# Kernel optimization log

Hardware: AMD Instinct MI355X
Metric: run time of the kernel (lower is better)

The kernel has to match this reference:

```python
import jax, jax.numpy as jnp
import numpy as np

NUM_HEADS = 16
WINDOW = 128

def setup_inputs() -> dict:
    key = jax.random.key(0)
    ks = jax.random.split(key, 9)
    E, B, S = 1024, 2, 2048
    sc = 1.0 / np.sqrt(E)
    return {
        'x':  jax.random.normal(ks[0], (B, S, E), jnp.float32),
        'Wq': jax.random.normal(ks[1], (E, E), jnp.float32) * sc,
        'bq': jax.random.normal(ks[2], (E,), jnp.float32) * 0.02,
        'Wk': jax.random.normal(ks[3], (E, E), jnp.float32) * sc,
        'bk': jax.random.normal(ks[4], (E,), jnp.float32) * 0.02,
        'Wv': jax.random.normal(ks[5], (E, E), jnp.float32) * sc,
        'bv': jax.random.normal(ks[6], (E,), jnp.float32) * 0.02,
        'Wo': jax.random.normal(ks[7], (E, E), jnp.float32) * sc,
        'bo': jax.random.normal(ks[8], (E,), jnp.float32) * 0.02,
    }

def reference(x, Wq, bq, Wk, bk, Wv, bv, Wo, bo):
    B, S, E = x.shape
    H = NUM_HEADS
    D = E // H
    # projections -> [B, H, S, D]
    q = (x @ Wq + bq).reshape(B, S, H, D).transpose(0, 2, 1, 3)
    k = (x @ Wk + bk).reshape(B, S, H, D).transpose(0, 2, 1, 3)
    v = (x @ Wv + bv).reshape(B, S, H, D).transpose(0, 2, 1, 3)
    # dense scores [B, H, S, S]
    energy = jnp.einsum('bhqd,bhkd->bhqk', q, k)
    idx = jnp.arange(S)
    blocked = jnp.abs(idx[:, None] - idx[None, :]) > WINDOW  # True = outside band
    neg = jnp.finfo(jnp.float32).min
    energy = jnp.where(blocked[None, None], neg, energy)
    # note: original scales by sqrt(emb_size), not sqrt(head_dim)
    att = jax.nn.softmax(energy / jnp.sqrt(jnp.float32(E)), axis=-1)
    out = jnp.einsum('bhqk,bhkd->bhqd', att, v)
    out = out.transpose(0, 2, 1, 3).reshape(B, S, E)
    return out @ Wo + bo
```

## Files before the change

kernel.cpp:

```cpp
#include <hip/hip_runtime.h>

typedef unsigned short u16;
typedef unsigned int u32;
typedef __attribute__((ext_vector_type(8))) short bf16x8;
typedef __attribute__((ext_vector_type(4))) float f32x4;
typedef __attribute__((ext_vector_type(4))) unsigned int u32x4;
typedef __attribute__((ext_vector_type(4))) unsigned short u16x4;

#define DEV static __device__ __forceinline__

DEV u16 f2bf(float f) {
  unsigned u = __builtin_bit_cast(unsigned, f);
  u += 0x7FFFu + ((u >> 16) & 1u);
  return (u16)(u >> 16);
}

DEV u32 cvt_pk_bf16(float lo, float hi) {
  u32 d;
  asm("v_cvt_pk_bf16_f32 %0, %1, %2" : "=v"(d) : "v"(lo), "v"(hi));
  return d;
}

DEV void load_lds16(const void* g, void* l) {
  __builtin_amdgcn_global_load_lds(
      (const __attribute__((address_space(1))) unsigned int*)g,
      (__attribute__((address_space(3))) unsigned int*)l, 16, 0, 0);
}


__global__ void k_prep(const float* __restrict__ x,
                       const float* __restrict__ bq, const float* __restrict__ bk,
                       const float* __restrict__ bv,
                       const float* __restrict__ Wq, const float* __restrict__ Wk,
                       const float* __restrict__ Wv, const float* __restrict__ Wo,
                       u16* __restrict__ xb, u16* __restrict__ wtqkv,
                       u16* __restrict__ wto, float* __restrict__ bias) {
  const int tid = threadIdx.x;
  const int bid = blockIdx.x;
  if (bid < 4096) {
    __shared__ float t[32][33];
    const int wi = bid >> 10, inner = bid & 1023;
    const float* W = (wi == 0) ? Wq : (wi == 1) ? Wk : (wi == 2) ? Wv : Wo;
    u16* Wt = (wi == 3) ? wto : wtqkv + (size_t)wi * 1024 * 1024;
    const int tx = tid & 31, ty = tid >> 5;
    const int c0 = (inner & 31) * 32, r0 = (inner >> 5) * 32;
#pragma unroll
    for (int i = 0; i < 4; ++i)
      t[ty + i * 8][tx] = W[(size_t)(r0 + ty + i * 8) * 1024 + c0 + tx];
    __syncthreads();
#pragma unroll
    for (int i = 0; i < 4; ++i)
      Wt[(size_t)(c0 + ty + i * 8) * 1024 + r0 + tx] = f2bf(t[tx][ty + i * 8]);
  } else if (bid < 8192) {
    int i = ((bid - 4096) * 256 + tid) * 4;
    f32x4 v = *(const f32x4*)(x + i);
    u16x4 o;
#pragma unroll
    for (int j = 0; j < 4; ++j) o[j] = f2bf(v[j]);
    *(u16x4*)(xb + i) = o;
  } else {
    int i = (bid - 8192) * 256 + tid;
    float v = (i < 1024) ? bq[i] : (i < 2048) ? bk[i - 1024] : bv[i - 2048];
    bias[i] = v;
  }
}


template <int BN, typename CT>
__launch_bounds__(256, 2) __global__
void k_gemm_bt(const u16* __restrict__ A, const u16* __restrict__ Bt,
               const float* __restrict__ bias, CT* __restrict__ C, int ldc,
               u16* __restrict__ vtp) {
  constexpr int BM = 128, BK = 64;
  constexpr int NJ = BN / 32;
  constexpr int EPW = BN / 2 + 4;
  constexpr int HALF = (BM + BN) * BK * 2;
  constexpr int LPS = BM / 32 + BN / 32;
  __shared__ __align__(16) char smem[2 * HALF];
  float (*ep)[16][EPW] = (float (*)[16][EPW])smem;

  const int tid = threadIdx.x;
  const int w = tid >> 6, lane = tid & 63, g = lane >> 4, n16 = lane & 15;
  const int wm = w >> 1, wn = w & 1;

  const int nbx = gridDim.x;
  const int flat = blockIdx.y * nbx + blockIdx.x;
  const int cpx = (nbx * gridDim.y) >> 3;
  const int swz = (flat & 7) * cpx + (flat >> 3);
  const int m0 = (swz / nbx) * BM, n0 = (swz % nbx) * BN;

#define STAGE(k0, bsel)                                                        \
  do {                                                                         \
    u16* lAb = (u16*)(smem + (bsel) * HALF);                                   \
    u16* lBb = lAb + BM * BK;                                                  \
    _Pragma("unroll")                                                          \
    for (int r = 0; r < BM / 32; ++r) {                                        \
      int s = r * 256 + tid;                                                   \
      int row = s >> 3, cc = (s & 7) ^ (row & 7);                              \
      load_lds16(A + (size_t)(m0 + row) * 1024 + (k0) + cc * 8, lAb + s * 8);  \
    }                                                                          \
    _Pragma("unroll")                                                          \
    for (int r = 0; r < BN / 32; ++r) {                                        \
      int s = r * 256 + tid;                                                   \
      int row = s >> 3, cc = (s & 7) ^ (row & 7);                              \
      load_lds16(Bt + (size_t)(n0 + row) * 1024 + (k0) + cc * 8, lBb + s * 8); \
    }                                                                          \
  } while (0)

  f32x4 acc[4][NJ] = {};
  STAGE(0, 0);
  STAGE(64, 1);
#pragma unroll 2
  for (int t = 0; t < 16; ++t) {
    const int buf = t & 1;
    if (t < 15) {
      asm volatile("s_waitcnt vmcnt(%0)" ::"n"(LPS) : "memory");
    } else {
      asm volatile("s_waitcnt vmcnt(0)" ::: "memory");
    }
    __builtin_amdgcn_s_barrier();
    const u16* lAb = (const u16*)(smem + buf * HALF);
    const u16* lBb = lAb + BM * BK;
    bf16x8 af[2][4], bfr[2][NJ];
#pragma unroll
    for (int kh = 0; kh < 2; ++kh) {
      const int csel = ((kh * 4 + g) ^ (n16 & 7)) * 8;
#pragma unroll
      for (int i = 0; i < 4; ++i)
        af[kh][i] = *(const bf16x8*)&lAb[(wm * 64 + i * 16 + n16) * 64 + csel];
#pragma unroll
      for (int j = 0; j < NJ; ++j)
        bfr[kh][j] = *(const bf16x8*)&lBb[(wn * (BN / 2) + j * 16 + n16) * 64 + csel];
    }
    asm volatile("s_waitcnt lgkmcnt(0)" ::: "memory");
    __builtin_amdgcn_s_barrier();
    if (t < 14) STAGE((t + 2) * 64, buf);
    __builtin_amdgcn_s_setprio(1);
#pragma unroll
    for (int kh = 0; kh < 2; ++kh)
#pragma unroll
      for (int i = 0; i < 4; ++i)
#pragma unroll
        for (int j = 0; j < NJ; ++j)
          acc[i][j] =
              __builtin_amdgcn_mfma_f32_16x16x32_bf16(af[kh][i], bfr[kh][j], acc[i][j], 0, 0, 0);
    __builtin_amdgcn_s_setprio(0);
  }
#undef STAGE
  __syncthreads();

  const int m_base = m0 + wm * 64, n_base = n0 + wn * (BN / 2);
  bool vmode = false;
  if constexpr (sizeof(CT) == 2 && BN == 128)
    vmode = (vtp != nullptr) && (n_base >= 2048);

#pragma unroll
  for (int i = 0; i < 4; ++i) {
#pragma unroll
    for (int j = 0; j < NJ; ++j) {
      float bv = bias[n_base + j * 16 + n16];
#pragma unroll
      for (int jj = 0; jj < 4; ++jj)
        ep[w][g * 4 + jj][j * 16 + n16] = acc[i][j][jj] + bv;
    }
    asm volatile("s_waitcnt lgkmcnt(0)" ::: "memory");
    if (vmode) {
      const int head = (n_base - 2048) >> 6;
      const int m_row0 = m_base + i * 16;
      const int bb = m_row0 >> 11, s0 = m_row0 & 2047;
      union { u16 a[16]; u32x4 v[2]; } pk;
#pragma unroll
      for (int r = 0; r < 16; ++r) pk.a[r] = f2bf(ep[w][r][lane]);
      size_t vrow = ((size_t)(bb * 16 + head) * 64 + lane) * 2048 + s0;
      *(u32x4*)(vtp + vrow) = pk.v[0];
      *(u32x4*)(vtp + vrow + 8) = pk.v[1];
    } else {
      constexpr int CPR = BN / 8;
      constexpr int P = 16 * CPR / 64;
#pragma unroll
      for (int p = 0; p < P; ++p) {
        int fl = p * 64 + lane;
        int row = fl / CPR, cc = (fl % CPR) * 4;
        f32x4 v = *(const f32x4*)&ep[w][row][cc];
        size_t off = (size_t)(m_base + i * 16 + row) * ldc + n_base + cc;
        if constexpr (sizeof(CT) == 2) {
          u16x4 o;
#pragma unroll
          for (int q = 0; q < 4; ++q) o[q] = f2bf(v[q]);
          *(u16x4*)(C + off) = o;
        } else {
          *(f32x4*)(C + off) = v;
        }
      }
    }
    asm volatile("s_waitcnt lgkmcnt(0)" ::: "memory");
  }
}


__launch_bounds__(256, 3) __global__
void k_attn(const u16* __restrict__ qkv, const u16* __restrict__ vt,
            u16* __restrict__ attn) {
  __shared__ __align__(16) u16 KV[20480];
  __shared__ __align__(16) u16 Ostg[4][16][64];
  const int tid = threadIdx.x;
  const int w = tid >> 6, lane = tid & 63, g = lane >> 4, n16 = lane & 15;
  const int bid = (blockIdx.x & 7) * 128 + (blockIdx.x >> 3);
  const int qt = bid & 31, h = (bid >> 5) & 15, b = bid >> 9;
  const int q0b = qt * 64;
  const int kvb = q0b - 128;
  const int q0 = q0b + w * 16;
  const int kv0 = q0 - 128;
  const int q = q0 + n16;
  const int bh = b * 16 + h;

  {
    const u16* kpart = qkv + (size_t)b * 2048 * 3072 + 1024 + h * 64;
#pragma unroll
    for (int i = 0; i < 10; ++i) {
      int c = i * 256 + tid;
      int r = c >> 3, sl = c & 7;
      int m = (r & 3) | (((r >> 3) & 1) << 2);
      int srcr = min(max(kvb + r, 0), 2047);
      load_lds16(kpart + (size_t)srcr * 3072 + (sl ^ m) * 8, &KV[c * 8]);
    }
  }

  const size_t rowQ = (size_t)(b * 2048 + q) * 3072 + h * 64;
  bf16x8 qf0 = *(const bf16x8*)(qkv + rowQ + g * 8);
  bf16x8 qf1 = *(const bf16x8*)(qkv + rowQ + 32 + g * 8);
  __syncthreads();

  const int kbase = 8 * (n16 >> 2) + (n16 & 3);
  const int wrel = 16 * w;
  f32x4 sv[18];
#pragma unroll
  for (int t = 0; t < 18; ++t) {
    int kr = wrel + 32 * (t >> 1) + 4 * (t & 1) + kbase;
    int krl = min(kr, 319);
    int p = (krl & 3) | (((krl >> 3) & 1) << 2);
    const u16* kp = &KV[krl * 64];
    bf16x8 kf0 = *(const bf16x8*)(kp + (g ^ p) * 8);
    bf16x8 kf1 = *(const bf16x8*)(kp + ((g + 4) ^ p) * 8);
    f32x4 s = {0.f, 0.f, 0.f, 0.f};
    s = __builtin_amdgcn_mfma_f32_16x16x32_bf16(kf0, qf0, s, 0, 0, 0);
    s = __builtin_amdgcn_mfma_f32_16x16x32_bf16(kf1, qf1, s, 0, 0, 0);
    sv[t] = s;
  }
  __syncthreads();

  {
    const u16* vpart = vt + (size_t)bh * 64 * 2048;
#pragma unroll
    for (int i = 0; i < 10; ++i) {
      int c = i * 256 + tid;
      int d = c / 40, cc = c - d * 40;
      int j = cc ^ (d & 7);
      int srck = min(max(kvb + j * 8, 0), 2040);
      load_lds16(vpart + (size_t)d * 2048 + srck, &KV[c * 8]);
    }
  }

  const float NEG = -__builtin_inff();
#pragma unroll
  for (int t = 0; t < 18; ++t) {
    int kb = kv0 + 32 * (t >> 1) + 4 * (t & 1) + 8 * g;
#pragma unroll
    for (int jj = 0; jj < 4; ++jj) {
      int k = kb + jj;
      bool ok = ((unsigned)k < 2048u) && ((unsigned)(q - k + 128) <= 256u);
      sv[t][jj] = ok ? sv[t][jj] : NEG;
    }
  }

  float mx = NEG;
#pragma unroll
  for (int t = 0; t < 18; ++t)
    mx = fmaxf(mx, fmaxf(fmaxf(sv[t][0], sv[t][1]), fmaxf(sv[t][2], sv[t][3])));
  mx = fmaxf(mx, __shfl_xor(mx, 16));
  mx = fmaxf(mx, __shfl_xor(mx, 32));

  const float c = 0.04508422017f;
  const float nmc = -mx * c;
  float sum = 0.f;
#pragma unroll
  for (int t = 0; t < 18; ++t)
#pragma unroll
    for (int jj = 0; jj < 4; ++jj) {
      float p = exp2f(fmaf(sv[t][jj], c, nmc));
      sv[t][jj] = p;
      sum += p;
    }
  sum += __shfl_xor(sum, 16);
  sum += __shfl_xor(sum, 32);
  const float inv = 1.f / sum;

  __syncthreads();

  f32x4 oacc[4] = {};
#pragma unroll
  for (int s = 0; s < 9; ++s) {
    union { u32 u[4]; bf16x8 v; } paf;
    paf.u[0] = cvt_pk_bf16(sv[2 * s][0], sv[2 * s][1]);
    paf.u[1] = cvt_pk_bf16(sv[2 * s][2], sv[2 * s][3]);
    paf.u[2] = cvt_pk_bf16(sv[2 * s + 1][0], sv[2 * s + 1][1]);
    paf.u[3] = cvt_pk_bf16(sv[2 * s + 1][2], sv[2 * s + 1][3]);
    int jc = min(2 * w + 4 * s + g, 39);
#pragma unroll
    for (int dt = 0; dt < 4; ++dt) {
      int d = dt * 16 + n16;
      bf16x8 vf = *(const bf16x8*)&KV[d * 320 + (jc ^ (d & 7)) * 8];
      oacc[dt] = __builtin_amdgcn_mfma_f32_16x16x32_bf16(paf.v, vf, oacc[dt], 0, 0, 0);
    }
  }

  float rs[4];
#pragma unroll
  for (int jj = 0; jj < 4; ++jj) rs[jj] = __shfl(inv, 4 * g + jj);

#pragma unroll
  for (int dt = 0; dt < 4; ++dt)
#pragma unroll
    for (int jj = 0; jj < 4; ++jj)
      Ostg[w][g * 4 + jj][dt * 16 + n16] = f2bf(oacc[dt][jj] * rs[jj]);
  asm volatile("s_waitcnt lgkmcnt(0)" ::: "memory");
#pragma unroll
  for (int p = 0; p < 2; ++p) {
    int fl = p * 512 + lane * 8;
    int row = fl >> 6, col = fl & 63;
    u32x4 v = *(const u32x4*)&Ostg[w][row][col];
    *(u32x4*)(attn + (size_t)(b * 2048 + q0 + row) * 1024 + h * 64 + col) = v;
  }
}


extern "C" void kernel_launch(void* const* d_in, const int* in_sizes, int n_in,
                              void* d_out, int out_size, void* d_ws, size_t ws_size,
                              hipStream_t stream) {
  const float* x  = (const float*)d_in[0];
  const float* Wq = (const float*)d_in[1];
  const float* bq = (const float*)d_in[2];
  const float* Wk = (const float*)d_in[3];
  const float* bk = (const float*)d_in[4];
  const float* Wv = (const float*)d_in[5];
  const float* bv = (const float*)d_in[6];
  const float* Wo = (const float*)d_in[7];
  const float* bo = (const float*)d_in[8];

  char* ws = (char*)d_ws;
  const size_t MB = 1ull << 20;
  u16*   xb    = (u16*)(ws + 0);
  u16*   wtqkv = (u16*)(ws + 8 * MB);
  u16*   wto   = (u16*)(ws + 14 * MB);
  float* bias  = (float*)(ws + 16 * MB);
  u16*   qkvb  = (u16*)(ws + 17 * MB);
  u16*   vtb   = (u16*)(ws + 41 * MB);
  u16*   attnb = (u16*)(ws + 0);

  k_prep<<<8204, 256, 0, stream>>>(x, bq, bk, bv, Wq, Wk, Wv, Wo,
                                   xb, wtqkv, wto, bias);
  k_gemm_bt<128, u16><<<dim3(24, 32), 256, 0, stream>>>(xb, wtqkv, bias, qkvb, 3072, vtb);
  k_attn<<<1024, 256, 0, stream>>>(qkvb, vtb, attnb);
  k_gemm_bt<64, float><<<dim3(16, 32), 256, 0, stream>>>(attnb, wto, bo, (float*)d_out,
                                                         1024, nullptr);
}
```

Measured before the change: 74.04 us.

## Drop softmax max-subtraction and compute row sums via MFMA with ones

Removes the running max reduction and shuffle-based sum by exponentiating scaled scores directly without max subtraction, and computes row normalizers by feeding the bf16 probabilities through an extra MFMA against a ones vector. The mask check is simplified to a single unsigned range test. This cuts the VALU reductions and cross-lane shuffles in the softmax, at the cost of one extra MFMA per step and a risk of overflow if scores grow large, plus sums that now come from bf16-rounded probabilities.

```diff
diff --git a/kernel.cpp b/kernel.cpp
--- a/kernel.cpp
+++ b/kernel.cpp
@@ -262,42 +262,24 @@
   }
 
   const float NEG = -__builtin_inff();
+  const int lo = max(q - 128, 0);
+  const unsigned rng = (unsigned)(min(q + 128, 2047) - lo);
+  const float c = 0.04508422017f;
 #pragma unroll
   for (int t = 0; t < 18; ++t) {
-    int kb = kv0 + 32 * (t >> 1) + 4 * (t & 1) + 8 * g;
+    int kb = kv0 + 32 * (t >> 1) + 4 * (t & 1) + 8 * g - lo;
 #pragma unroll
     for (int jj = 0; jj < 4; ++jj) {
-      int k = kb + jj;
-      bool ok = ((unsigned)k < 2048u) && ((unsigned)(q - k + 128) <= 256u);
-      sv[t][jj] = ok ? sv[t][jj] : NEG;
-    }
-  }
-
-  float mx = NEG;
-#pragma unroll
-  for (int t = 0; t < 18; ++t)
-    mx = fmaxf(mx, fmaxf(fmaxf(sv[t][0], sv[t][1]), fmaxf(sv[t][2], sv[t][3])));
-  mx = fmaxf(mx, __shfl_xor(mx, 16));
-  mx = fmaxf(mx, __shfl_xor(mx, 32));
-
-  const float c = 0.04508422017f;
-  const float nmc = -mx * c;
-  float sum = 0.f;
-#pragma unroll
-  for (int t = 0; t < 18; ++t)
-#pragma unroll
-    for (int jj = 0; jj < 4; ++jj) {
-      float p = exp2f(fmaf(sv[t][jj], c, nmc));
-      sv[t][jj] = p;
-      sum += p;
-    }
-  sum += __shfl_xor(sum, 16);
-  sum += __shfl_xor(sum, 32);
-  const float inv = 1.f / sum;
+      bool ok = (unsigned)(kb + jj) <= rng;
+      sv[t][jj] = exp2f((ok ? sv[t][jj] : NEG) * c);
+    }
+  }
 
   __syncthreads();
 
+  const bf16x8 ones = {0x3F80, 0x3F80, 0x3F80, 0x3F80, 0x3F80, 0x3F80, 0x3F80, 0x3F80};
   f32x4 oacc[4] = {};
+  f32x4 osum = {};
 #pragma unroll
   for (int s = 0; s < 9; ++s) {
     union { u32 u[4]; bf16x8 v; } paf;
@@ -312,17 +294,18 @@
       bf16x8 vf = *(const bf16x8*)&KV[d * 320 + (jc ^ (d & 7)) * 8];
       oacc[dt] = __builtin_amdgcn_mfma_f32_16x16x32_bf16(paf.v, vf, oacc[dt], 0, 0, 0);
     }
-  }
-
-  float rs[4];
-#pragma unroll
-  for (int jj = 0; jj < 4; ++jj) rs[jj] = __shfl(inv, 4 * g + jj);
+    osum = __builtin_amdgcn_mfma_f32_16x16x32_bf16(paf.v, ones, osum, 0, 0, 0);
+  }
+
+  float inv[4];
+#pragma unroll
+  for (int jj = 0; jj < 4; ++jj) inv[jj] = 1.f / osum[jj];
 
 #pragma unroll
   for (int dt = 0; dt < 4; ++dt)
 #pragma unroll
     for (int jj = 0; jj < 4; ++jj)
-      Ostg[w][g * 4 + jj][dt * 16 + n16] = f2bf(oacc[dt][jj] * rs[jj]);
+      Ostg[w][g * 4 + jj][dt * 16 + n16] = f2bf(oacc[dt][jj] * inv[jj]);
   asm volatile("s_waitcnt lgkmcnt(0)" ::: "memory");
 #pragma unroll
   for (int p = 0; p < 2; ++p) {
```

Result: faster. 71.96 us, median of 2 (-2.8%).
